# Kernel tuning notes

Measured on AMD Instinct MI355X. Metric: run time of the kernel, lower is better.

## Reference

```python
import jax, jax.numpy as jnp
import numpy as np

INPUT_SIZE = 64
HIDDEN = 16
BATCH = 1048576


def setup_inputs() -> dict:
    key = jax.random.key(0)
    ks = jax.random.split(key, 16)
    D = INPUT_SIZE + HIDDEN
    s = 1.0 / np.sqrt(D)  # torch nn.Linear default init scale
    inp = {
        "x": jax.random.normal(ks[0], (BATCH, INPUT_SIZE), jnp.float32),
        "h_prev": jax.random.normal(ks[1], (BATCH, HIDDEN), jnp.float32),
        "c_prev": jax.random.normal(ks[2], (BATCH, HIDDEN), jnp.float32),
        "delta_t": jax.random.uniform(ks[3], (BATCH,), jnp.float32),
    }
    names = ["i", "f", "o", "c", "d"]
    for j, n in enumerate(names):
        inp[f"W_{n}"] = jax.random.uniform(ks[4 + 2 * j], (D, HIDDEN), jnp.float32, -s, s)
        inp[f"b_{n}"] = jax.random.uniform(ks[5 + 2 * j], (HIDDEN,), jnp.float32, -s, s)
    return inp


def reference(x, h_prev, c_prev, delta_t, W_i, b_i, W_f, b_f, W_o, b_o, W_c, b_c, W_d, b_d):
    combined = jnp.concatenate([x, h_prev], axis=1)  # [B, D]
    # Fuse the five small GEMMs into one [D, 5H] GEMM (same math).
    W = jnp.concatenate([W_i, W_f, W_o, W_c, W_d], axis=1)  # [D, 5H]
    b = jnp.concatenate([b_i, b_f, b_o, b_c, b_d])  # [5H]
    z = combined @ W + b  # [B, 5H]
    zi, zf, zo, zc, zd = jnp.split(z, 5, axis=1)
    i = jnp.tanh(zi)
    f = jnp.tanh(zf)
    o = jnp.tanh(zo)
    c_tilde = jnp.tanh(zc)
    decay = jax.nn.softplus(zd)
    c_decay = c_prev * jnp.exp(-decay * delta_t[:, None])
    c_next = f * c_decay + i * c_tilde
    h_next = o * jnp.tanh(c_next)
    return (h_next, c_next)
```

## Files before the change

kernel.cpp:

```cpp
#include <hip/hip_runtime.h>


#define BATCH   1048576
#define NTILES  (BATCH / 16)
#define L2E     1.442695041f
#define LN2     0.6931471806f

typedef __bf16 bf16x8 __attribute__((ext_vector_type(8)));
typedef float  f32x4  __attribute__((ext_vector_type(4)));

#define WS_BIAS_OFF 15360

__device__ __forceinline__ float fast_tanh(float x) {
    float e = __builtin_amdgcn_exp2f(x * (2.0f * L2E));
    return 1.0f - 2.0f * __builtin_amdgcn_rcpf(e + 1.0f);
}

__global__ void pack_w_kernel(const float* __restrict__ Wi, const float* __restrict__ bi,
                              const float* __restrict__ Wf, const float* __restrict__ bf_,
                              const float* __restrict__ Wo, const float* __restrict__ bo,
                              const float* __restrict__ Wc, const float* __restrict__ bc,
                              const float* __restrict__ Wd, const float* __restrict__ bd,
                              void* __restrict__ ws)
{
    const float* W[5]  = {Wi, Wf, Wo, Wc, Wd};
    const float* BP[5] = {bi, bf_, bo, bc, bd};
    const int b    = blockIdx.x;
    const int lane = threadIdx.x;
    if (b < 15) {
        const int t = b / 3, kt = b % 3;
        const int quad = lane >> 4, col = lane & 15;
        bf16x8 f;
        #pragma unroll
        for (int j = 0; j < 8; ++j) {
            int k = kt * 32 + quad * 8 + j;
            float v = (k < 80) ? W[t][k * 16 + col] : 0.0f;
            f[j] = (__bf16)v;
        }
        ((bf16x8*)ws)[b * 64 + lane] = f;
    } else {
        if (lane < 80) {
            int t = lane >> 4, col = lane & 15;
            ((float*)((char*)ws + WS_BIAS_OFF))[lane] = BP[t][col];
        }
    }
}

__global__ __launch_bounds__(256, 4)
void ctlstm_kernel(const float* __restrict__ x,
                   const float* __restrict__ hprev,
                   const float* __restrict__ cprev,
                   const float* __restrict__ dt,
                   const void* __restrict__ ws,
                   float* __restrict__ out)
{
    const int lane = threadIdx.x & 63;
    const int col  = lane & 15;
    const int quad = lane >> 4;

    const bf16x8* wsfrag = (const bf16x8*)ws;
    const float*  wsbias = (const float*)((const char*)ws + WS_BIAS_OFF);
    bf16x8 Bfrag[3][5];
    float  biasv[5];
    #pragma unroll
    for (int t = 0; t < 5; ++t) {
        biasv[t] = wsbias[t * 16 + col];
        #pragma unroll
        for (int kt = 0; kt < 3; ++kt)
            Bfrag[kt][t] = wsfrag[(t * 3 + kt) * 64 + lane];
    }

    const int nwaves = (gridDim.x * blockDim.x) >> 6;
    const int gw     = (blockIdx.x * blockDim.x + threadIdx.x) >> 6;

    const float4* X4 = (const float4*)x;
    const float4* H4 = (const float4*)hprev;

    for (int tile = gw; tile < NTILES; tile += nwaves) {
        const int rowbase = tile << 4;
        const int arow    = rowbase + col;

        float4 a0 = X4[arow * 16 + quad * 2];
        float4 a1 = X4[arow * 16 + quad * 2 + 1];
        float4 a2 = X4[arow * 16 + 8 + quad * 2];
        float4 a3 = X4[arow * 16 + 8 + quad * 2 + 1];
        float4 a4 = make_float4(0.f, 0.f, 0.f, 0.f);
        float4 a5 = make_float4(0.f, 0.f, 0.f, 0.f);
        if (quad < 2) {
            a4 = H4[arow * 4 + quad * 2];
            a5 = H4[arow * 4 + quad * 2 + 1];
        }

        float cp[4], dtv[4];
        #pragma unroll
        for (int r = 0; r < 4; ++r) {
            const int row = rowbase + quad * 4 + r;
            cp[r]  = cprev[row * 16 + col];
            dtv[r] = dt[row];
        }

        bf16x8 A0, A1, A2;
        #pragma unroll
        for (int j = 0; j < 4; ++j) {
            A0[j]     = (__bf16)((const float*)&a0)[j];
            A0[j + 4] = (__bf16)((const float*)&a1)[j];
            A1[j]     = (__bf16)((const float*)&a2)[j];
            A1[j + 4] = (__bf16)((const float*)&a3)[j];
            A2[j]     = (__bf16)((const float*)&a4)[j];
            A2[j + 4] = (__bf16)((const float*)&a5)[j];
        }

        f32x4 acc[5];
        #pragma unroll
        for (int t = 0; t < 5; ++t) {
            f32x4 c0 = {biasv[t], biasv[t], biasv[t], biasv[t]};
            c0 = __builtin_amdgcn_mfma_f32_16x16x32_bf16(A0, Bfrag[0][t], c0, 0, 0, 0);
            c0 = __builtin_amdgcn_mfma_f32_16x16x32_bf16(A1, Bfrag[1][t], c0, 0, 0, 0);
            acc[t] = __builtin_amdgcn_mfma_f32_16x16x32_bf16(A2, Bfrag[2][t], c0, 0, 0, 0);
        }

        #pragma unroll
        for (int r = 0; r < 4; ++r) {
            const int row = rowbase + quad * 4 + r;

            float zi = acc[0][r], zf = acc[1][r], zo = acc[2][r];
            float zc = acc[3][r], zd = acc[4][r];

            float i_g = fast_tanh(zi);
            float f_g = fast_tanh(zf);
            float o_g = fast_tanh(zo);
            float ctl = fast_tanh(zc);

            float ax = fabsf(zd);
            float e  = __builtin_amdgcn_exp2f(-ax * L2E);
            float sp = fmaxf(zd, 0.0f) + __builtin_amdgcn_logf(1.0f + e) * LN2;

            float cdec = cp[r] * __builtin_amdgcn_exp2f(-sp * dtv[r] * L2E);
            float cn   = f_g * cdec + i_g * ctl;
            float hn   = o_g * fast_tanh(cn);

            __builtin_nontemporal_store(hn, &out[row * 16 + col]);
            __builtin_nontemporal_store(cn, &out[BATCH * 16 + row * 16 + col]);
        }
    }
}

extern "C" void kernel_launch(void* const* d_in, const int* in_sizes, int n_in,
                              void* d_out, int out_size, void* d_ws, size_t ws_size,
                              hipStream_t stream) {
    pack_w_kernel<<<16, 64, 0, stream>>>(
        (const float*)d_in[4],  (const float*)d_in[5],
        (const float*)d_in[6],  (const float*)d_in[7],
        (const float*)d_in[8],  (const float*)d_in[9],
        (const float*)d_in[10], (const float*)d_in[11],
        (const float*)d_in[12], (const float*)d_in[13],
        d_ws);
    ctlstm_kernel<<<8192, 256, 0, stream>>>(
        (const float*)d_in[0], (const float*)d_in[1],
        (const float*)d_in[2], (const float*)d_in[3],
        d_ws, (float*)d_out);
}
```

Baseline: 508.8 us.

## Swap MFMA operands for row-contiguous outputs, stage weights in LDS, prefetch both tiles

Operands of the MFMA are swapped so each lane owns one batch row and four consecutive hidden columns. This allows 16-byte vectorized loads of c_prev and the bias, and vectorized nontemporal stores of h and c instead of scalar strided accesses. Packed weights are copied into shared memory per block and read from LDS at use time rather than held in registers. The grid-stride loop is replaced by exactly two tiles per wave, with all global loads for both issued up front to raise memory-level parallelism. This adds an LDS copy and barrier per block and hard-codes the grid size to the batch.

Measured after the change: 503.7 us. About the same (-1.0%).

```diff
diff --git a/kernel.cpp b/kernel.cpp
--- a/kernel.cpp
+++ b/kernel.cpp
@@ -3,6 +3,8 @@
 
 #define BATCH   1048576
 #define NTILES  (BATCH / 16)
+#define NBLOCKS 8192
+#define NWAVES  (NBLOCKS * 4)
 #define L2E     1.442695041f
 #define LN2     0.6931471806f
 
@@ -10,6 +12,7 @@
 typedef float  f32x4  __attribute__((ext_vector_type(4)));
 
 #define WS_BIAS_OFF 15360
+#define WS_BYTES    15680
 
 __device__ __forceinline__ float fast_tanh(float x) {
     float e = __builtin_amdgcn_exp2f(x * (2.0f * L2E));
@@ -54,75 +57,90 @@
                    const void* __restrict__ ws,
                    float* __restrict__ out)
 {
-    const int lane = threadIdx.x & 63;
+    __shared__ __align__(16) char smem[WS_BYTES];
+    const int tid = threadIdx.x;
+
+    {
+        const float4* src = (const float4*)ws;
+        float4*       dst = (float4*)smem;
+        #pragma unroll
+        for (int i = 0; i < 4; ++i) {
+            int idx = tid + i * 256;
+            if (idx < WS_BYTES / 16) dst[idx] = src[idx];
+        }
+    }
+    __syncthreads();
+
+    const int lane = tid & 63;
     const int col  = lane & 15;
     const int quad = lane >> 4;
 
-    const bf16x8* wsfrag = (const bf16x8*)ws;
-    const float*  wsbias = (const float*)((const char*)ws + WS_BIAS_OFF);
-    bf16x8 Bfrag[3][5];
-    float  biasv[5];
+    float4 b4[5];
     #pragma unroll
-    for (int t = 0; t < 5; ++t) {
-        biasv[t] = wsbias[t * 16 + col];
-        #pragma unroll
-        for (int kt = 0; kt < 3; ++kt)
-            Bfrag[kt][t] = wsfrag[(t * 3 + kt) * 64 + lane];
-    }
+    for (int t = 0; t < 5; ++t)
+        b4[t] = *(const float4*)(smem + WS_BIAS_OFF + t * 64 + quad * 16);
 
-    const int nwaves = (gridDim.x * blockDim.x) >> 6;
-    const int gw     = (blockIdx.x * blockDim.x + threadIdx.x) >> 6;
+    const int gw = (blockIdx.x * 256 + tid) >> 6;
 
     const float4* X4 = (const float4*)x;
     const float4* H4 = (const float4*)hprev;
+    const float4* C4 = (const float4*)cprev;
 
-    for (int tile = gw; tile < NTILES; tile += nwaves) {
-        const int rowbase = tile << 4;
-        const int arow    = rowbase + col;
+    const int arow0 = (gw << 4) + col;
+    const int arow1 = ((gw + NWAVES) << 4) + col;
 
-        float4 a0 = X4[arow * 16 + quad * 2];
-        float4 a1 = X4[arow * 16 + quad * 2 + 1];
-        float4 a2 = X4[arow * 16 + 8 + quad * 2];
-        float4 a3 = X4[arow * 16 + 8 + quad * 2 + 1];
-        float4 a4 = make_float4(0.f, 0.f, 0.f, 0.f);
-        float4 a5 = make_float4(0.f, 0.f, 0.f, 0.f);
-        if (quad < 2) {
-            a4 = H4[arow * 4 + quad * 2];
-            a5 = H4[arow * 4 + quad * 2 + 1];
-        }
+    float4 a0 = X4[arow0 * 16 + quad * 2];
+    float4 a1 = X4[arow0 * 16 + quad * 2 + 1];
+    float4 a2 = X4[arow0 * 16 + quad * 2 + 8];
+    float4 a3 = X4[arow0 * 16 + quad * 2 + 9];
+    float4 cv0 = C4[arow0 * 4 + quad];
+    float  dv0 = dt[arow0];
 
-        float cp[4], dtv[4];
-        #pragma unroll
-        for (int r = 0; r < 4; ++r) {
-            const int row = rowbase + quad * 4 + r;
-            cp[r]  = cprev[row * 16 + col];
-            dtv[r] = dt[row];
-        }
+    float4 g0 = X4[arow1 * 16 + quad * 2];
+    float4 g1 = X4[arow1 * 16 + quad * 2 + 1];
+    float4 g2 = X4[arow1 * 16 + quad * 2 + 8];
+    float4 g3 = X4[arow1 * 16 + quad * 2 + 9];
+    float4 cv1 = C4[arow1 * 4 + quad];
+    float  dv1 = dt[arow1];
 
+    float4 a4 = make_float4(0.f, 0.f, 0.f, 0.f), a5 = a4;
+    float4 g4 = a4, g5 = a4;
+    if (quad < 2) {
+        a4 = H4[arow0 * 4 + quad * 2];
+        a5 = H4[arow0 * 4 + quad * 2 + 1];
+        g4 = H4[arow1 * 4 + quad * 2];
+        g5 = H4[arow1 * 4 + quad * 2 + 1];
+    }
+
+    const bf16x8* WF = (const bf16x8*)smem;
+
+    auto process = [&](int arow,
+                       const float4& p0, const float4& p1, const float4& p2,
+                       const float4& p3, const float4& p4, const float4& p5,
+                       const float4& cp4, float dtv) {
         bf16x8 A0, A1, A2;
         #pragma unroll
         for (int j = 0; j < 4; ++j) {
-            A0[j]     = (__bf16)((const float*)&a0)[j];
-            A0[j + 4] = (__bf16)((const float*)&a1)[j];
-            A1[j]     = (__bf16)((const float*)&a2)[j];
-            A1[j + 4] = (__bf16)((const float*)&a3)[j];
-            A2[j]     = (__bf16)((const float*)&a4)[j];
-            A2[j + 4] = (__bf16)((const float*)&a5)[j];
+            A0[j]     = (__bf16)((const float*)&p0)[j];
+            A0[j + 4] = (__bf16)((const float*)&p1)[j];
+            A1[j]     = (__bf16)((const float*)&p2)[j];
+            A1[j + 4] = (__bf16)((const float*)&p3)[j];
+            A2[j]     = (__bf16)((const float*)&p4)[j];
+            A2[j + 4] = (__bf16)((const float*)&p5)[j];
         }
 
         f32x4 acc[5];
         #pragma unroll
         for (int t = 0; t < 5; ++t) {
-            f32x4 c0 = {biasv[t], biasv[t], biasv[t], biasv[t]};
-            c0 = __builtin_amdgcn_mfma_f32_16x16x32_bf16(A0, Bfrag[0][t], c0, 0, 0, 0);
-            c0 = __builtin_amdgcn_mfma_f32_16x16x32_bf16(A1, Bfrag[1][t], c0, 0, 0, 0);
-            acc[t] = __builtin_amdgcn_mfma_f32_16x16x32_bf16(A2, Bfrag[2][t], c0, 0, 0, 0);
+            f32x4 c0 = {b4[t].x, b4[t].y, b4[t].z, b4[t].w};
+            c0 = __builtin_amdgcn_mfma_f32_16x16x32_bf16(WF[(t * 3 + 0) * 64 + lane], A0, c0, 0, 0, 0);
+            c0 = __builtin_amdgcn_mfma_f32_16x16x32_bf16(WF[(t * 3 + 1) * 64 + lane], A1, c0, 0, 0, 0);
+            acc[t] = __builtin_amdgcn_mfma_f32_16x16x32_bf16(WF[(t * 3 + 2) * 64 + lane], A2, c0, 0, 0, 0);
         }
 
+        f32x4 hn4, cn4;
         #pragma unroll
         for (int r = 0; r < 4; ++r) {
-            const int row = rowbase + quad * 4 + r;
-
             float zi = acc[0][r], zf = acc[1][r], zo = acc[2][r];
             float zc = acc[3][r], zd = acc[4][r];
 
@@ -135,14 +153,19 @@
             float e  = __builtin_amdgcn_exp2f(-ax * L2E);
             float sp = fmaxf(zd, 0.0f) + __builtin_amdgcn_logf(1.0f + e) * LN2;
 
-            float cdec = cp[r] * __builtin_amdgcn_exp2f(-sp * dtv[r] * L2E);
+            float cdec = ((const float*)&cp4)[r] * __builtin_amdgcn_exp2f(-sp * dtv * L2E);
             float cn   = f_g * cdec + i_g * ctl;
             float hn   = o_g * fast_tanh(cn);
 
-            __builtin_nontemporal_store(hn, &out[row * 16 + col]);
-            __builtin_nontemporal_store(cn, &out[BATCH * 16 + row * 16 + col]);
+            hn4[r] = hn;
+            cn4[r] = cn;
         }
-    }
+        __builtin_nontemporal_store(hn4, (f32x4*)(out + (size_t)arow * 16 + quad * 4));
+        __builtin_nontemporal_store(cn4, (f32x4*)(out + (size_t)BATCH * 16 + (size_t)arow * 16 + quad * 4));
+    };
+
+    process(arow0, a0, a1, a2, a3, a4, a5, cv0, dv0);
+    process(arow1, g0, g1, g2, g3, g4, g5, cv1, dv1);
 }
 
 extern "C" void kernel_launch(void* const* d_in, const int* in_sizes, int n_in,
@@ -155,7 +178,7 @@
         (const float*)d_in[10], (const float*)d_in[11],
         (const float*)d_in[12], (const float*)d_in[13],
         d_ws);
-    ctlstm_kernel<<<8192, 256, 0, stream>>>(
+    ctlstm_kernel<<<NBLOCKS, 256, 0, stream>>>(
         (const float*)d_in[0], (const float*)d_in[1],
         (const float*)d_in[2], (const float*)d_in[3],
         d_ws, (float*)d_out);
```
